# Kernel tuning notes

Hardware: AMD Instinct MI355X
Metric: run time of the kernel (lower is better)

Reference implementation:

```python
import jax, jax.numpy as jnp
import numpy as np

EPS_ATTN = 1e-6
EPS_LN = 1e-5


def _layer_norm(x, g, b):
    m = jnp.mean(x, axis=-1, keepdims=True)
    v = jnp.mean((x - m) ** 2, axis=-1, keepdims=True)
    return (x - m) * jax.lax.rsqrt(v + EPS_LN) * g + b


def _linear_attention(q, k, v):
    # q,k,v: [N, L/S, H, D]; elu feature map (+1 keeps values positive)
    q = jax.nn.elu(q) + 1.0
    k = jax.nn.elu(k) + 1.0
    s_len = v.shape[1]
    v = v / s_len
    kv = jnp.einsum('nshd,nshv->nhdv', k, v)            # [N,H,D,D]
    z = 1.0 / (jnp.einsum('nlhd,nhd->nlh', q, k.sum(axis=1)) + EPS_ATTN)
    out = jnp.einsum('nlhd,nhdv->nlhv', q, kv) * z[..., None] * s_len
    return out


def setup_inputs() -> dict:
    key = jax.random.key(0)
    ks = jax.random.split(key, 8)
    N, L, S, H, D = 4, 4096, 4096, 8, 64
    sc = 0.05
    return {
        'x': jax.random.normal(ks[0], (N, L, H, D), jnp.float32),
        'source': jax.random.normal(ks[1], (N, S, H, D), jnp.float32),
        'wq': jax.random.normal(ks[2], (D, D), jnp.float32) * sc,
        'wk': jax.random.normal(ks[3], (D, D), jnp.float32) * sc,
        'wv': jax.random.normal(ks[4], (D, D), jnp.float32) * sc,
        'wmerge': jax.random.normal(ks[5], (D, D), jnp.float32) * sc,
        'w1': jax.random.normal(ks[6], (2 * D, 2 * D), jnp.float32) * sc,
        'w2': jax.random.normal(ks[7], (D, 2 * D), jnp.float32) * sc,
        'g1': jnp.ones((D,), jnp.float32),
        'b1': jnp.zeros((D,), jnp.float32),
        'g2': jnp.ones((D,), jnp.float32),
        'b2': jnp.zeros((D,), jnp.float32),
    }


def reference(x, source, wq, wk, wv, wmerge, w1, w2, g1, b1, g2, b2):
    # projections (torch Linear: y = x @ W.T), applied on last dim D=d_model
    q = jnp.einsum('nlhd,ed->nlhe', x, wq)
    k = jnp.einsum('nshd,ed->nshe', source, wk)
    v = jnp.einsum('nshd,ed->nshe', source, wv)
    message = _linear_attention(q, k, v)                # [N,L,H,D]
    message = jnp.einsum('nlhd,ed->nlhe', message, wmerge)
    message = _layer_norm(message, g1, b1)
    h = jnp.concatenate([x, message], axis=-1)          # [N,L,H,2D]
    h = jax.nn.relu(jnp.einsum('nlhd,ed->nlhe', h, w1))
    h = jnp.einsum('nlhd,ed->nlhe', h, w2)              # [N,L,H,D]
    h = _layer_norm(h, g2, b2)
    return x + h
```

## Files before the change

### kernel.cpp

```cpp
#include <hip/hip_runtime.h>
#include <cstdint>

#define NB 4
#define LL 4096
#define SS 4096
#define HH 8
#define DD 64
#define NHC (NB*HH)

typedef unsigned short ushort_t;
typedef __bf16 bf16x8 __attribute__((ext_vector_type(8)));
typedef float f32x4 __attribute__((ext_vector_type(4)));
typedef unsigned short u16x8 __attribute__((ext_vector_type(8)));

__device__ __forceinline__ float bf2f(unsigned short u) {
    union { unsigned int i; float f; } v; v.i = ((unsigned int)u) << 16; return v.f;
}
__device__ __forceinline__ unsigned short f2bf(float f) {
    union { float ff; unsigned int i; } v; v.ff = f;
    unsigned int x = v.i;
    x += 0x7fffu + ((x >> 16) & 1u);
    return (unsigned short)(x >> 16);
}
__device__ __forceinline__ bool input_is_bf16(const void* g1) {
    return ((const unsigned short*)g1)[0] == 0x3F80u;
}

template<bool BF16>
__device__ __forceinline__ float ldgf(const void* p, size_t i) {
    if constexpr (BF16) return bf2f(((const unsigned short*)p)[i]);
    else                return ((const float*)p)[i];
}
template<bool BF16>
__device__ __forceinline__ u16x8 ld8(const void* p, size_t i) {
    if constexpr (BF16) {
        return *reinterpret_cast<const u16x8*>((const unsigned short*)p + i);
    } else {
        const float* f = (const float*)p + i;
        u16x8 o;
        #pragma unroll
        for (int j = 0; j < 8; ++j) o[j] = f2bf(f[j]);
        return o;
    }
}
__device__ __forceinline__ bf16x8 ldsA(const ushort_t* p) {
    return *reinterpret_cast<const bf16x8*>(p);
}
#define MFMA16(a,b,c) __builtin_amdgcn_mfma_f32_16x16x32_bf16(a,b,c,0,0,0)

template<bool BF16, int LC>
__device__ __forceinline__ void stage_w(const void* g, size_t goff, ushort_t* dst,
                                        int rows, int dstride, int tid) {
    int total8 = (rows << LC) >> 3;
    for (int i8 = tid; i8 < total8; i8 += 256) {
        int i = i8 << 3;
        int r = i >> LC, c = i & ((1 << LC) - 1);
        *reinterpret_cast<u16x8*>(dst + r * dstride + c) = ld8<BF16>(g, goff + i);
    }
}

__device__ __forceinline__ void red16(float v[4]) {
    #pragma unroll
    for (int m = 1; m < 16; m <<= 1) {
        #pragma unroll
        for (int r = 0; r < 4; ++r) v[r] += __shfl_xor(v[r], m);
    }
}

template<bool BF16>
__device__ void kv_body(const void* __restrict__ src, const void* __restrict__ wk,
                        const void* __restrict__ wv, float* __restrict__ kvg,
                        float* __restrict__ ksumg,
                        ushort_t* S, ushort_t* KT, ushort_t* VT)
{
    const int tid = threadIdx.x;
    const int lane = tid & 63, w = tid >> 6;
    const int lg = lane >> 4, l15 = lane & 15;
    const int bid = blockIdx.x;
    const int nh = bid >> 3, ch = bid & 7;
    const int n = nh >> 3, h = nh & 7;
    const int s0 = ch * 512;
    const f32x4 z4 = {0.f, 0.f, 0.f, 0.f};

    stage_w<BF16, 6>(wk, 0, KT, 64, 136, tid);
    stage_w<BF16, 6>(wv, 0, VT, 64, 136, tid);
    __syncthreads();
    bf16x8 wkf[2][4], wvf[2][4];
    #pragma unroll
    for (int ks = 0; ks < 2; ++ks)
        #pragma unroll
        for (int nt = 0; nt < 4; ++nt) {
            wkf[ks][nt] = ldsA(KT + (nt * 16 + l15) * 136 + ks * 32 + lg * 8);
            wvf[ks][nt] = ldsA(VT + (nt * 16 + l15) * 136 + ks * 32 + lg * 8);
        }
    __syncthreads();

    f32x4 kvacc[4];
    #pragma unroll
    for (int nt = 0; nt < 4; ++nt) kvacc[nt] = z4;
    float ksp[4] = {0.f, 0.f, 0.f, 0.f};

    for (int st = 0; st < 4; ++st) {
        for (int i = tid; i < 128 * 8; i += 256) {
            int r = i >> 3, c8 = (i & 7) << 3;
            size_t gb = ((size_t)((size_t)n * SS + (s0 + st * 128 + r)) * HH + h) * DD + c8;
            *reinterpret_cast<u16x8*>(S + r * 72 + c8) = ld8<BF16>(src, gb);
        }
        __syncthreads();

        #pragma unroll
        for (int mtt = 0; mtt < 2; ++mtt) {
            const int rowA = w * 32 + mtt * 16;
            bf16x8 af[2];
            #pragma unroll
            for (int ks = 0; ks < 2; ++ks)
                af[ks] = ldsA(S + (rowA + l15) * 72 + ks * 32 + lg * 8);
            f32x4 ka[4], va[4];
            #pragma unroll
            for (int nt = 0; nt < 4; ++nt) { ka[nt] = z4; va[nt] = z4; }
            #pragma unroll
            for (int ks = 0; ks < 2; ++ks)
                #pragma unroll
                for (int nt = 0; nt < 4; ++nt) {
                    ka[nt] = MFMA16(af[ks], wkf[ks][nt], ka[nt]);
                    va[nt] = MFMA16(af[ks], wvf[ks][nt], va[nt]);
                }
            #pragma unroll
            for (int nt = 0; nt < 4; ++nt)
                #pragma unroll
                for (int r = 0; r < 4; ++r) {
                    float kvl = ka[nt][r];
                    kvl = kvl > 0.f ? kvl + 1.f : __expf(kvl);
                    ksp[nt] += kvl;
                    int srow = rowA + lg * 4 + r;
                    int dcol = nt * 16 + l15;
                    KT[dcol * 136 + srow] = f2bf(kvl);
                    VT[dcol * 136 + srow] = f2bf(va[nt][r]);
                }
        }
        __syncthreads();

        #pragma unroll
        for (int ks = 0; ks < 4; ++ks) {
            bf16x8 akv = ldsA(KT + (w * 16 + l15) * 136 + ks * 32 + lg * 8);
            #pragma unroll
            for (int nt = 0; nt < 4; ++nt) {
                bf16x8 bkv = ldsA(VT + (nt * 16 + l15) * 136 + ks * 32 + lg * 8);
                kvacc[nt] = MFMA16(akv, bkv, kvacc[nt]);
            }
        }
        __syncthreads();
    }

    float* kvo = kvg + (size_t)nh * DD * DD;
    #pragma unroll
    for (int nt = 0; nt < 4; ++nt)
        #pragma unroll
        for (int r = 0; r < 4; ++r)
            atomicAdd(&kvo[(w * 16 + lg * 4 + r) * DD + nt * 16 + l15], kvacc[nt][r]);
    #pragma unroll
    for (int m = 16; m < 64; m <<= 1)
        #pragma unroll
        for (int nt = 0; nt < 4; ++nt) ksp[nt] += __shfl_xor(ksp[nt], m);
    if (lane < 16) {
        #pragma unroll
        for (int nt = 0; nt < 4; ++nt)
            atomicAdd(&ksumg[nh * DD + nt * 16 + lane], ksp[nt]);
    }
}

__global__ __launch_bounds__(256, 2) void kv_kernel(
    const void* __restrict__ src, const void* __restrict__ wk, const void* __restrict__ wv,
    const void* __restrict__ g1, float* __restrict__ kvg, float* __restrict__ ksumg)
{
    __shared__ ushort_t S[128 * 72];
    __shared__ ushort_t KT[64 * 136];
    __shared__ ushort_t VT[64 * 136];
    if (input_is_bf16(g1)) kv_body<true >(src, wk, wv, kvg, ksumg, S, KT, VT);
    else                   kv_body<false>(src, wk, wv, kvg, ksumg, S, KT, VT);
}

template<bool BF16>
__device__ void main_body(const void* __restrict__ x,
                          const void* __restrict__ wq, const void* __restrict__ wm,
                          const void* __restrict__ w1, const void* __restrict__ w2,
                          const void* __restrict__ g1, const void* __restrict__ b1,
                          const void* __restrict__ g2, const void* __restrict__ b2,
                          const float* __restrict__ kvg, const float* __restrict__ ksumg,
                          void* __restrict__ outp,
                          ushort_t* w1s, ushort_t* kvs, ushort_t* B0, ushort_t* B1,
                          ushort_t* B2)
{
    const int tid = threadIdx.x;
    const int lane = tid & 63, w = tid >> 6;
    const int lg = lane >> 4, l15 = lane & 15;
    const int bid = blockIdx.x;
    const int nh = bid >> 4, ch = bid & 15;
    const int n = nh >> 3, h = nh & 7;
    const int rowA = w * 16;
    const f32x4 z4 = {0.f, 0.f, 0.f, 0.f};

    stage_w<BF16, 6>(wq, 0, B0, 64, 72, tid);
    stage_w<BF16, 6>(wm, 0, B1, 64, 72, tid);
    stage_w<BF16, 7>(w2, 0, w1s, 64, 136, tid);
    for (int i = tid; i < 4096; i += 256) {
        int d = i >> 6, e = i & 63;
        B2[d * 72 + e] = f2bf(kvg[(size_t)nh * 4096 + i]);
    }
    __syncthreads();

    bf16x8 wqf[2][4], w2f[4][4];
    #pragma unroll
    for (int ks = 0; ks < 2; ++ks)
        #pragma unroll
        for (int nt = 0; nt < 4; ++nt)
            wqf[ks][nt] = ldsA(B0 + (nt * 16 + l15) * 72 + ks * 32 + lg * 8);
    #pragma unroll
    for (int ks = 0; ks < 4; ++ks)
        #pragma unroll
        for (int nt = 0; nt < 4; ++nt)
            w2f[ks][nt] = ldsA(w1s + (nt * 16 + l15) * 136 + ks * 32 + lg * 8);
    {
        bf16x8 akv[2];
        #pragma unroll
        for (int ks = 0; ks < 2; ++ks)
            akv[ks] = ldsA(B2 + (w * 16 + l15) * 72 + ks * 32 + lg * 8);
        f32x4 km[4];
        #pragma unroll
        for (int nt = 0; nt < 4; ++nt) km[nt] = z4;
        #pragma unroll
        for (int ks = 0; ks < 2; ++ks)
            #pragma unroll
            for (int nt = 0; nt < 4; ++nt) {
                bf16x8 bwm = ldsA(B1 + (nt * 16 + l15) * 72 + ks * 32 + lg * 8);
                km[nt] = MFMA16(akv[ks], bwm, km[nt]);
            }
        #pragma unroll
        for (int nt = 0; nt < 4; ++nt)
            #pragma unroll
            for (int r = 0; r < 4; ++r)
                kvs[(nt * 16 + l15) * 72 + w * 16 + lg * 4 + r] = f2bf(km[nt][r]);
    }
    __syncthreads();

    stage_w<BF16, 7>(w1, 0, w1s, 128, 136, tid);
    bf16x8 kvmf[2][4];
    #pragma unroll
    for (int ks = 0; ks < 2; ++ks)
        #pragma unroll
        for (int nt = 0; nt < 4; ++nt)
            kvmf[ks][nt] = ldsA(kvs + (nt * 16 + l15) * 72 + ks * 32 + lg * 8);
    float g1r[4], b1r[4], g2r[4], b2r[4], ksr[4];
    #pragma unroll
    for (int nt = 0; nt < 4; ++nt) {
        int c = nt * 16 + l15;
        g1r[nt] = ldgf<BF16>(g1, c); b1r[nt] = ldgf<BF16>(b1, c);
        g2r[nt] = ldgf<BF16>(g2, c); b2r[nt] = ldgf<BF16>(b2, c);
        ksr[nt] = ksumg[nh * 64 + c];
    }
    __syncthreads();

    for (int t = 0; t < 4; ++t) {
        const int l0 = ch * 256 + t * 64;

        #pragma unroll
        for (int p = 0; p < 2; ++p) {
            int r16 = p * 8 + (lane >> 3), c8 = (lane & 7) << 3;
            size_t gb = ((size_t)((size_t)n * LL + (l0 + rowA + r16)) * HH + h) * DD + c8;
            *reinterpret_cast<u16x8*>(B0 + (rowA + r16) * 72 + c8) = ld8<BF16>(x, gb);
        }

        bf16x8 af[2];
        #pragma unroll
        for (int ks = 0; ks < 2; ++ks)
            af[ks] = ldsA(B0 + (rowA + l15) * 72 + ks * 32 + lg * 8);
        f32x4 qa[4];
        #pragma unroll
        for (int nt = 0; nt < 4; ++nt) qa[nt] = z4;
        #pragma unroll
        for (int ks = 0; ks < 2; ++ks)
            #pragma unroll
            for (int nt = 0; nt < 4; ++nt)
                qa[nt] = MFMA16(af[ks], wqf[ks][nt], qa[nt]);
        float zp[4] = {0.f, 0.f, 0.f, 0.f};
        #pragma unroll
        for (int nt = 0; nt < 4; ++nt)
            #pragma unroll
            for (int r = 0; r < 4; ++r) {
                float v = qa[nt][r];
                v = v > 0.f ? v + 1.f : __expf(v);
                zp[r] += v * ksr[nt];
                B1[(rowA + lg * 4 + r) * 72 + nt * 16 + l15] = f2bf(v);
            }
        red16(zp);
        float zr[4];
        #pragma unroll
        for (int r = 0; r < 4; ++r) zr[r] = 1.f / (zp[r] + 1e-6f);

        #pragma unroll
        for (int ks = 0; ks < 2; ++ks)
            af[ks] = ldsA(B1 + (rowA + l15) * 72 + ks * 32 + lg * 8);
        f32x4 ma[4];
        #pragma unroll
        for (int nt = 0; nt < 4; ++nt) ma[nt] = z4;
        #pragma unroll
        for (int ks = 0; ks < 2; ++ks)
            #pragma unroll
            for (int nt = 0; nt < 4; ++nt)
                ma[nt] = MFMA16(af[ks], kvmf[ks][nt], ma[nt]);
        #pragma unroll
        for (int nt = 0; nt < 4; ++nt)
            #pragma unroll
            for (int r = 0; r < 4; ++r) ma[nt][r] *= zr[r];

        float s1[4] = {0.f,0.f,0.f,0.f}, s2[4] = {0.f,0.f,0.f,0.f};
        #pragma unroll
        for (int nt = 0; nt < 4; ++nt)
            #pragma unroll
            for (int r = 0; r < 4; ++r) {
                float v = ma[nt][r]; s1[r] += v; s2[r] += v * v;
            }
        red16(s1); red16(s2);
        #pragma unroll
        for (int r = 0; r < 4; ++r) {
            float mu = s1[r] * 0.015625f;
            float var = s2[r] * 0.015625f - mu * mu;
            s1[r] = mu; s2[r] = rsqrtf(var + 1e-5f);
        }
        #pragma unroll
        for (int nt = 0; nt < 4; ++nt)
            #pragma unroll
            for (int r = 0; r < 4; ++r)
                B1[(rowA + lg * 4 + r) * 72 + nt * 16 + l15] =
                    f2bf((ma[nt][r] - s1[r]) * s2[r] * g1r[nt] + b1r[nt]);

        f32x4 ha[4];
        #pragma unroll
        for (int nt = 0; nt < 4; ++nt) ha[nt] = z4;
        #pragma unroll
        for (int half = 0; half < 2; ++half) {
            f32x4 ta[4];
            #pragma unroll
            for (int nt = 0; nt < 4; ++nt) ta[nt] = z4;
            #pragma unroll
            for (int ks = 0; ks < 4; ++ks) {
                const ushort_t* bp = (ks < 2) ? B0 : B1;
                bf16x8 a1 = ldsA(bp + (rowA + l15) * 72 + (ks & 1) * 32 + lg * 8);
                #pragma unroll
                for (int nt = 0; nt < 4; ++nt) {
                    bf16x8 bw = ldsA(w1s + (half * 64 + nt * 16 + l15) * 136 + ks * 32 + lg * 8);
                    ta[nt] = MFMA16(a1, bw, ta[nt]);
                }
            }
            #pragma unroll
            for (int nt = 0; nt < 4; ++nt)
                #pragma unroll
                for (int r = 0; r < 4; ++r)
                    B2[(rowA + lg * 4 + r) * 72 + nt * 16 + l15] =
                        f2bf(fmaxf(ta[nt][r], 0.f));
            #pragma unroll
            for (int k2 = 0; k2 < 2; ++k2) {
                bf16x8 a2 = ldsA(B2 + (rowA + l15) * 72 + k2 * 32 + lg * 8);
                #pragma unroll
                for (int nt = 0; nt < 4; ++nt)
                    ha[nt] = MFMA16(a2, w2f[half * 2 + k2][nt], ha[nt]);
            }
        }

        float t1[4] = {0.f,0.f,0.f,0.f}, t2[4] = {0.f,0.f,0.f,0.f};
        #pragma unroll
        for (int nt = 0; nt < 4; ++nt)
            #pragma unroll
            for (int r = 0; r < 4; ++r) {
                float v = ha[nt][r]; t1[r] += v; t2[r] += v * v;
            }
        red16(t1); red16(t2);
        #pragma unroll
        for (int r = 0; r < 4; ++r) {
            float mu = t1[r] * 0.015625f;
            float var = t2[r] * 0.015625f - mu * mu;
            t1[r] = mu; t2[r] = rsqrtf(var + 1e-5f);
        }
        #pragma unroll
        for (int nt = 0; nt < 4; ++nt)
            #pragma unroll
            for (int r = 0; r < 4; ++r) {
                float xv = bf2f(B0[(rowA + lg * 4 + r) * 72 + nt * 16 + l15]);
                float ov = xv + (ha[nt][r] - t1[r]) * t2[r] * g2r[nt] + b2r[nt];
                B1[(rowA + lg * 4 + r) * 72 + nt * 16 + l15] = f2bf(ov);
            }

        #pragma unroll
        for (int p = 0; p < 2; ++p) {
            int r16 = p * 8 + (lane >> 3), c8 = (lane & 7) << 3;
            size_t gb = ((size_t)((size_t)n * LL + (l0 + rowA + r16)) * HH + h) * DD + c8;
            u16x8 v = *reinterpret_cast<const u16x8*>(B1 + (rowA + r16) * 72 + c8);
            if constexpr (BF16) {
                *reinterpret_cast<u16x8*>((unsigned short*)outp + gb) = v;
            } else {
                float* fo = (float*)outp + gb;
                #pragma unroll
                for (int j = 0; j < 8; ++j) fo[j] = bf2f(v[j]);
            }
        }
    }
}

__global__ __launch_bounds__(256, 2) void main_kernel(
    const void* __restrict__ x,
    const void* __restrict__ wq, const void* __restrict__ wm,
    const void* __restrict__ w1, const void* __restrict__ w2,
    const void* __restrict__ g1, const void* __restrict__ b1,
    const void* __restrict__ g2, const void* __restrict__ b2,
    const float* __restrict__ kvg, const float* __restrict__ ksumg,
    void* __restrict__ outp)
{
    __shared__ ushort_t w1s[128 * 136];
    __shared__ ushort_t kvs[64 * 72];
    __shared__ ushort_t B0[64 * 72];
    __shared__ ushort_t B1[64 * 72];
    __shared__ ushort_t B2[64 * 72];
    if (input_is_bf16(g1))
        main_body<true >(x, wq, wm, w1, w2, g1, b1, g2, b2, kvg, ksumg, outp,
                         w1s, kvs, B0, B1, B2);
    else
        main_body<false>(x, wq, wm, w1, w2, g1, b1, g2, b2, kvg, ksumg, outp,
                         w1s, kvs, B0, B1, B2);
}

extern "C" void kernel_launch(void* const* d_in, const int* in_sizes, int n_in,
                              void* d_out, int out_size, void* d_ws, size_t ws_size,
                              hipStream_t stream) {
    const void* x   = d_in[0];
    const void* src = d_in[1];
    const void* wq  = d_in[2];
    const void* wk  = d_in[3];
    const void* wv  = d_in[4];
    const void* wm  = d_in[5];
    const void* w1  = d_in[6];
    const void* w2  = d_in[7];
    const void* g1  = d_in[8];
    const void* b1  = d_in[9];
    const void* g2  = d_in[10];
    const void* b2  = d_in[11];

    float* kvg   = (float*)d_ws;
    float* ksumg = kvg + (size_t)NHC * DD * DD;

    hipMemsetAsync(d_ws, 0, ((size_t)NHC * DD * DD + NHC * DD) * sizeof(float), stream);
    kv_kernel<<<NHC * 8, 256, 0, stream>>>(src, wk, wv, g1, kvg, ksumg);
    main_kernel<<<NHC * 16, 256, 0, stream>>>(x, wq, wm, w1, w2, g1, b1, g2, b2,
                                              kvg, ksumg, d_out);
}
```

Measured before the change: 164.8 us.

## Split KV reduction across more blocks and prefetch x rows in main kernel

The kv kernel now launches four times as many blocks, each handling one 128-row source chunk instead of looping over four. This removes the per-iteration barriers and exposes more parallelism, at the cost of more atomic adds into the shared kv accumulator. KT/VT transposed stores become 4-wide vector writes, and the occupancy hint is raised to 3. In the main kernel, the next tile of x is loaded into registers before compute so global latency overlaps with the matmuls, and MFMA sections are wrapped in setprio raises.

After: 171.0 us. 3.8% more time.

```diff
diff --git a/kernel.cpp b/kernel.cpp
--- a/kernel.cpp
+++ b/kernel.cpp
@@ -12,6 +12,7 @@
 typedef __bf16 bf16x8 __attribute__((ext_vector_type(8)));
 typedef float f32x4 __attribute__((ext_vector_type(4)));
 typedef unsigned short u16x8 __attribute__((ext_vector_type(8)));
+typedef unsigned short u16x4 __attribute__((ext_vector_type(4)));
 
 __device__ __forceinline__ float bf2f(unsigned short u) {
     union { unsigned int i; float f; } v; v.i = ((unsigned int)u) << 16; return v.f;
@@ -77,14 +78,20 @@
     const int lane = tid & 63, w = tid >> 6;
     const int lg = lane >> 4, l15 = lane & 15;
     const int bid = blockIdx.x;
-    const int nh = bid >> 3, ch = bid & 7;
+    const int nh = bid >> 5, ch = bid & 31;
     const int n = nh >> 3, h = nh & 7;
-    const int s0 = ch * 512;
+    const int s0 = ch * 128;
     const f32x4 z4 = {0.f, 0.f, 0.f, 0.f};
 
     stage_w<BF16, 6>(wk, 0, KT, 64, 136, tid);
     stage_w<BF16, 6>(wv, 0, VT, 64, 136, tid);
-    __syncthreads();
+    for (int i = tid; i < 128 * 8; i += 256) {
+        int r = i >> 3, c8 = (i & 7) << 3;
+        size_t gb = ((size_t)((size_t)n * SS + (s0 + r)) * HH + h) * DD + c8;
+        *reinterpret_cast<u16x8*>(S + r * 72 + c8) = ld8<BF16>(src, gb);
+    }
+    __syncthreads();
+
     bf16x8 wkf[2][4], wvf[2][4];
     #pragma unroll
     for (int ks = 0; ks < 2; ++ks)
@@ -95,61 +102,53 @@
         }
     __syncthreads();
 
+    float ksp[4] = {0.f, 0.f, 0.f, 0.f};
+    #pragma unroll
+    for (int mtt = 0; mtt < 2; ++mtt) {
+        const int rowA = w * 32 + mtt * 16;
+        bf16x8 af[2];
+        #pragma unroll
+        for (int ks = 0; ks < 2; ++ks)
+            af[ks] = ldsA(S + (rowA + l15) * 72 + ks * 32 + lg * 8);
+        f32x4 ka[4], va[4];
+        #pragma unroll
+        for (int nt = 0; nt < 4; ++nt) { ka[nt] = z4; va[nt] = z4; }
+        #pragma unroll
+        for (int ks = 0; ks < 2; ++ks)
+            #pragma unroll
+            for (int nt = 0; nt < 4; ++nt) {
+                ka[nt] = MFMA16(af[ks], wkf[ks][nt], ka[nt]);
+                va[nt] = MFMA16(af[ks], wvf[ks][nt], va[nt]);
+            }
+        #pragma unroll
+        for (int nt = 0; nt < 4; ++nt) {
+            u16x4 kp, vp;
+            #pragma unroll
+            for (int r = 0; r < 4; ++r) {
+                float kvl = ka[nt][r];
+                kvl = kvl > 0.f ? kvl + 1.f : __expf(kvl);
+                ksp[nt] += kvl;
+                kp[r] = f2bf(kvl);
+                vp[r] = f2bf(va[nt][r]);
+            }
+            const int dcol = nt * 16 + l15;
+            *reinterpret_cast<u16x4*>(KT + dcol * 136 + rowA + lg * 4) = kp;
+            *reinterpret_cast<u16x4*>(VT + dcol * 136 + rowA + lg * 4) = vp;
+        }
+    }
+    __syncthreads();
+
     f32x4 kvacc[4];
     #pragma unroll
     for (int nt = 0; nt < 4; ++nt) kvacc[nt] = z4;
-    float ksp[4] = {0.f, 0.f, 0.f, 0.f};
-
-    for (int st = 0; st < 4; ++st) {
-        for (int i = tid; i < 128 * 8; i += 256) {
-            int r = i >> 3, c8 = (i & 7) << 3;
-            size_t gb = ((size_t)((size_t)n * SS + (s0 + st * 128 + r)) * HH + h) * DD + c8;
-            *reinterpret_cast<u16x8*>(S + r * 72 + c8) = ld8<BF16>(src, gb);
-        }
-        __syncthreads();
-
-        #pragma unroll
-        for (int mtt = 0; mtt < 2; ++mtt) {
-            const int rowA = w * 32 + mtt * 16;
-            bf16x8 af[2];
-            #pragma unroll
-            for (int ks = 0; ks < 2; ++ks)
-                af[ks] = ldsA(S + (rowA + l15) * 72 + ks * 32 + lg * 8);
-            f32x4 ka[4], va[4];
-            #pragma unroll
-            for (int nt = 0; nt < 4; ++nt) { ka[nt] = z4; va[nt] = z4; }
-            #pragma unroll
-            for (int ks = 0; ks < 2; ++ks)
-                #pragma unroll
-                for (int nt = 0; nt < 4; ++nt) {
-                    ka[nt] = MFMA16(af[ks], wkf[ks][nt], ka[nt]);
-                    va[nt] = MFMA16(af[ks], wvf[ks][nt], va[nt]);
-                }
-            #pragma unroll
-            for (int nt = 0; nt < 4; ++nt)
-                #pragma unroll
-                for (int r = 0; r < 4; ++r) {
-                    float kvl = ka[nt][r];
-                    kvl = kvl > 0.f ? kvl + 1.f : __expf(kvl);
-                    ksp[nt] += kvl;
-                    int srow = rowA + lg * 4 + r;
-                    int dcol = nt * 16 + l15;
-                    KT[dcol * 136 + srow] = f2bf(kvl);
-                    VT[dcol * 136 + srow] = f2bf(va[nt][r]);
-                }
-        }
-        __syncthreads();
-
-        #pragma unroll
-        for (int ks = 0; ks < 4; ++ks) {
-            bf16x8 akv = ldsA(KT + (w * 16 + l15) * 136 + ks * 32 + lg * 8);
-            #pragma unroll
-            for (int nt = 0; nt < 4; ++nt) {
-                bf16x8 bkv = ldsA(VT + (nt * 16 + l15) * 136 + ks * 32 + lg * 8);
-                kvacc[nt] = MFMA16(akv, bkv, kvacc[nt]);
-            }
-        }
-        __syncthreads();
+    #pragma unroll
+    for (int ks = 0; ks < 4; ++ks) {
+        bf16x8 akv = ldsA(KT + (w * 16 + l15) * 136 + ks * 32 + lg * 8);
+        #pragma unroll
+        for (int nt = 0; nt < 4; ++nt) {
+            bf16x8 bkv = ldsA(VT + (nt * 16 + l15) * 136 + ks * 32 + lg * 8);
+            kvacc[nt] = MFMA16(akv, bkv, kvacc[nt]);
+        }
     }
 
     float* kvo = kvg + (size_t)nh * DD * DD;
@@ -169,7 +168,7 @@
     }
 }
 
-__global__ __launch_bounds__(256, 2) void kv_kernel(
+__global__ __launch_bounds__(256, 3) void kv_kernel(
     const void* __restrict__ src, const void* __restrict__ wk, const void* __restrict__ wv,
     const void* __restrict__ g1, float* __restrict__ kvg, float* __restrict__ ksumg)
 {
@@ -200,6 +199,18 @@
     const int rowA = w * 16;
     const f32x4 z4 = {0.f, 0.f, 0.f, 0.f};
 
+    auto ldx = [&](int t, u16x8 xv[2]) {
+        #pragma unroll
+        for (int p = 0; p < 2; ++p) {
+            int r16 = p * 8 + (lane >> 3), c8 = (lane & 7) << 3;
+            size_t gb = ((size_t)((size_t)n * LL + (ch * 256 + t * 64 + rowA + r16)) * HH + h) * DD + c8;
+            xv[p] = ld8<BF16>(x, gb);
+        }
+    };
+
+    u16x8 xv[2];
+    ldx(0, xv);
+
     stage_w<BF16, 6>(wq, 0, B0, 64, 72, tid);
     stage_w<BF16, 6>(wm, 0, B1, 64, 72, tid);
     stage_w<BF16, 7>(w2, 0, w1s, 64, 136, tid);
@@ -266,9 +277,10 @@
         #pragma unroll
         for (int p = 0; p < 2; ++p) {
             int r16 = p * 8 + (lane >> 3), c8 = (lane & 7) << 3;
-            size_t gb = ((size_t)((size_t)n * LL + (l0 + rowA + r16)) * HH + h) * DD + c8;
-            *reinterpret_cast<u16x8*>(B0 + (rowA + r16) * 72 + c8) = ld8<BF16>(x, gb);
-        }
+            *reinterpret_cast<u16x8*>(B0 + (rowA + r16) * 72 + c8) = xv[p];
+        }
+        u16x8 xn[2];
+        if (t < 3) ldx(t + 1, xn);
 
         bf16x8 af[2];
         #pragma unroll
@@ -277,11 +289,13 @@
         f32x4 qa[4];
         #pragma unroll
         for (int nt = 0; nt < 4; ++nt) qa[nt] = z4;
+        __builtin_amdgcn_s_setprio(1);
         #pragma unroll
         for (int ks = 0; ks < 2; ++ks)
             #pragma unroll
             for (int nt = 0; nt < 4; ++nt)
                 qa[nt] = MFMA16(af[ks], wqf[ks][nt], qa[nt]);
+        __builtin_amdgcn_s_setprio(0);
         float zp[4] = {0.f, 0.f, 0.f, 0.f};
         #pragma unroll
         for (int nt = 0; nt < 4; ++nt)
@@ -303,11 +317,13 @@
         f32x4 ma[4];
         #pragma unroll
         for (int nt = 0; nt < 4; ++nt) ma[nt] = z4;
+        __builtin_amdgcn_s_setprio(1);
         #pragma unroll
         for (int ks = 0; ks < 2; ++ks)
             #pragma unroll
             for (int nt = 0; nt < 4; ++nt)
                 ma[nt] = MFMA16(af[ks], kvmf[ks][nt], ma[nt]);
+        __builtin_amdgcn_s_setprio(0);
         #pragma unroll
         for (int nt = 0; nt < 4; ++nt)
             #pragma unroll
@@ -342,6 +358,7 @@
             f32x4 ta[4];
             #pragma unroll
             for (int nt = 0; nt < 4; ++nt) ta[nt] = z4;
+            __builtin_amdgcn_s_setprio(1);
             #pragma unroll
             for (int ks = 0; ks < 4; ++ks) {
                 const ushort_t* bp = (ks < 2) ? B0 : B1;
@@ -352,12 +369,14 @@
                     ta[nt] = MFMA16(a1, bw, ta[nt]);
                 }
             }
+            __builtin_amdgcn_s_setprio(0);
             #pragma unroll
             for (int nt = 0; nt < 4; ++nt)
                 #pragma unroll
                 for (int r = 0; r < 4; ++r)
                     B2[(rowA + lg * 4 + r) * 72 + nt * 16 + l15] =
                         f2bf(fmaxf(ta[nt][r], 0.f));
+            __builtin_amdgcn_s_setprio(1);
             #pragma unroll
             for (int k2 = 0; k2 < 2; ++k2) {
                 bf16x8 a2 = ldsA(B2 + (rowA + l15) * 72 + k2 * 32 + lg * 8);
@@ -365,6 +384,7 @@
                 for (int nt = 0; nt < 4; ++nt)
                     ha[nt] = MFMA16(a2, w2f[half * 2 + k2][nt], ha[nt]);
             }
+            __builtin_amdgcn_s_setprio(0);
         }
 
         float t1[4] = {0.f,0.f,0.f,0.f}, t2[4] = {0.f,0.f,0.f,0.f};
@@ -385,8 +405,8 @@
         for (int nt = 0; nt < 4; ++nt)
             #pragma unroll
             for (int r = 0; r < 4; ++r) {
-                float xv = bf2f(B0[(rowA + lg * 4 + r) * 72 + nt * 16 + l15]);
-                float ov = xv + (ha[nt][r] - t1[r]) * t2[r] * g2r[nt] + b2r[nt];
+                float xv2 = bf2f(B0[(rowA + lg * 4 + r) * 72 + nt * 16 + l15]);
+                float ov = xv2 + (ha[nt][r] - t1[r]) * t2[r] * g2r[nt] + b2r[nt];
                 B1[(rowA + lg * 4 + r) * 72 + nt * 16 + l15] = f2bf(ov);
             }
 
@@ -403,6 +423,8 @@
                 for (int j = 0; j < 8; ++j) fo[j] = bf2f(v[j]);
             }
         }
+
+        if (t < 3) { xv[0] = xn[0]; xv[1] = xn[1]; }
     }
 }
 
@@ -448,7 +470,7 @@
     float* ksumg = kvg + (size_t)NHC * DD * DD;
 
     hipMemsetAsync(d_ws, 0, ((size_t)NHC * DD * DD + NHC * DD) * sizeof(float), stream);
-    kv_kernel<<<NHC * 8, 256, 0, stream>>>(src, wk, wv, g1, kvg, ksumg);
+    kv_kernel<<<NHC * 32, 256, 0, stream>>>(src, wk, wv, g1, kvg, ksumg);
     main_kernel<<<NHC * 16, 256, 0, stream>>>(x, wq, wm, w1, w2, g1, b1, g2, b2,
                                               kvg, ksumg, d_out);
 }
```
